# Kernel optimization log

Hardware: AMD Instinct MI355X
Metric: run time of the kernel (lower is better)

The kernel has to match this reference:

```python
import jax, jax.numpy as jnp
import numpy as np

B, SE, HD, ED, N, T = 64, 512, 1024, 512, 10000, 20
EOS_ID = 1
NEG_BIG = -1e9    # stand-in for -MAX_VAL encoder pad mask
MASK_VAL = -1e7   # logits_mask scatter value (-10000000.0 in torch)
M = HD + ED


def setup_inputs() -> dict:
    key = jax.random.key(0)
    ks = jax.random.split(key, 16)
    s = 0.02
    enc = jax.random.normal(ks[0], (B, SE, HD), jnp.float32)
    hidden = jax.random.normal(ks[1], (1, B, HD), jnp.float32)
    cell = jax.random.normal(ks[2], (1, B, HD), jnp.float32)
    text_lengths = jax.random.randint(ks[3], (B,), SE // 2, SE + 1)
    encoder_mask = jnp.arange(SE)[None, :] < text_lengths[:, None]  # [B,SE] bool
    embedding = jax.random.normal(ks[4], (N, ED), jnp.float32) * s
    # LSTM (PyTorch gate order i,f,g,o)
    w_ih = jax.random.normal(ks[5], (4 * HD, ED), jnp.float32) * s
    w_hh = jax.random.normal(ks[6], (4 * HD, HD), jnp.float32) * s
    b_ih = jnp.zeros((4 * HD,), jnp.float32)
    b_hh = jnp.zeros((4 * HD,), jnp.float32)
    # dense_net: Hd -> He
    w_q = jax.random.normal(ks[7], (HD, HD), jnp.float32) * s
    b_q = jnp.zeros((HD,), jnp.float32)
    # SelfAttentiveSum: Linear(Ed,Ed)+ReLU+Linear(Ed,1)
    w_k = jax.random.normal(ks[8], (ED, ED), jnp.float32) * s
    b_k = jnp.zeros((ED,), jnp.float32)
    w_ko = jax.random.normal(ks[9], (ED,), jnp.float32) * s
    b_ko = jnp.zeros((), jnp.float32)
    # MLP: Linear(M,M)+ReLU+Linear(M,N)
    w_m1 = jax.random.normal(ks[10], (M, M), jnp.float32) * s
    b_m1 = jnp.zeros((M,), jnp.float32)
    w_m2 = jax.random.normal(ks[11], (N, M), jnp.float32) * s
    b_m2 = jnp.zeros((N,), jnp.float32)
    return dict(encoded_hidden_embeddings=enc, hidden=hidden, cell=cell,
                text_lengths=text_lengths, encoder_mask=encoder_mask,
                embedding=embedding, w_ih=w_ih, w_hh=w_hh, b_ih=b_ih, b_hh=b_hh,
                w_q=w_q, b_q=b_q, w_k=w_k, b_k=b_k, w_ko=w_ko, b_ko=b_ko,
                w_m1=w_m1, b_m1=b_m1, w_m2=w_m2, b_m2=b_m2)


def _decode(enc, h0, c0, encoder_mask, embedding, w_ih, w_hh, b_ih, b_hh,
            w_q, b_q, w_k, b_k, w_ko, b_ko, w_m1, b_m1, w_m2, b_m2):
    pad_mask = jnp.where(encoder_mask, 0.0, NEG_BIG).astype(enc.dtype)  # [B,SE]
    sent = enc[:, 0, :]  # [B,HD] sentence representation (dropout is identity in eval)

    def step(carry, t):
        h, c, inp, logits_mask, buf = carry
        # --- LSTM cell (single step) ---
        gates = inp @ w_ih.T + b_ih + h @ w_hh.T + b_hh  # [B,4HD]
        i, f, g, o = jnp.split(gates, 4, axis=-1)
        c = jax.nn.sigmoid(f) * c + jax.nn.sigmoid(i) * jnp.tanh(g)
        h = jax.nn.sigmoid(o) * jnp.tanh(c)
        # --- attention over encoder states ---
        q = h @ w_q.T + b_q                                   # [B,HD]
        score = jnp.einsum('bsh,bh->bs', enc, q) + pad_mask    # [B,SE]
        w = jax.nn.softmax(score, axis=1)
        attn_enc = jnp.einsum('bs,bsh->bh', w, enc)            # [B,HD]
        # --- self-attentive sum over previously predicted label embeddings ---
        valid = jnp.arange(T) < jnp.maximum(t, 1)              # step 0: zeros row 0 valid
        k = jax.nn.relu(buf @ w_k.T + b_k) @ w_ko + b_ko       # [B,T]
        k = jnp.where(valid[None, :], k, NEG_BIG)
        sw = jax.nn.softmax(k, axis=1)
        attn_last = jnp.einsum('bt,bte->be', sw, buf)          # [B,ED]
        # --- MLP ---
        m = jnp.concatenate([sent + attn_enc, inp + attn_last], axis=-1)  # [B,M]
        logits = jax.nn.relu(m @ w_m1.T + b_m1) @ w_m2.T + b_m2 + logits_mask  # [B,N]
        next_ids = jnp.argmax(logits, axis=-1)                 # [B]
        pred_emb = embedding[next_ids]                          # [B,ED]
        buf = buf.at[:, t].set(pred_emb)
        logits_mask = logits_mask.at[jnp.arange(B), next_ids].set(MASK_VAL)
        logits_mask = logits_mask.at[:, EOS_ID].set(0.0)
        return (h, c, pred_emb, logits_mask, buf), (logits, next_ids)

    init = (h0, c0,
            jnp.zeros((B, ED), enc.dtype),
            jnp.zeros((B, N), enc.dtype),
            jnp.zeros((B, T, ED), enc.dtype))
    _, (outs, ids) = jax.lax.scan(step, init, jnp.arange(T))
    return jnp.transpose(outs, (1, 0, 2)), jnp.transpose(ids, (1, 0))  # [B,T,N],[B,T]


def reference(encoded_hidden_embeddings, hidden, cell, text_lengths, encoder_mask,
              embedding, w_ih, w_hh, b_ih, b_hh, w_q, b_q, w_k, b_k, w_ko, b_ko,
              w_m1, b_m1, w_m2, b_m2):
    # De=1: [1,B,HD] -> [B,HD]
    return _decode(encoded_hidden_embeddings, hidden[0], cell[0], encoder_mask,
                   embedding, w_ih, w_hh, b_ih, b_hh, w_q, b_q, w_k, b_k,
                   w_ko, b_ko, w_m1, b_m1, w_m2, b_m2)
```

## Files before the change

kernel.cpp:

```cpp
#include <hip/hip_runtime.h>

#define B64 64
#define SE 512
#define HD 1024
#define ED 512
#define NV 10000
#define TT 20
#define MM 1536
#define MASK_VALF -10000000.0f

#define OFF_XA    0
#define OFF_XB    98304
#define OFF_CT    196608
#define OFF_QF    262144
#define OFF_FM    327680
#define OFF_FL    328704
#define OFF_FACC  329728
#define OFF_XT2   1378304
#define OFF_H1T   1476608
#define OFF_ARGV  1574912
#define OFF_ARGI  1654912
#define OFF_MASKT 1734912
#define OFF_BUF   2374912
#define OFF_BUFT  3030272
#define OFF_KVP   3685632
#define OFF_LP    3767552

__device__ __forceinline__ float sigmoidf_(float x) { return 1.f / (1.f + expf(-x)); }

__global__ __launch_bounds__(256) void k_init(const float* __restrict__ h0,
                                              const float* __restrict__ c0,
                                              float* __restrict__ ws) {
  int idx = blockIdx.x * 256 + threadIdx.x, stride = gridDim.x * 256;
  float* xa = ws + OFF_XA;
  float* cT = ws + OFF_CT;
  float* maskT = ws + OFF_MASKT;
  float* buf = ws + OFF_BUF;
  float* bufT = ws + OFF_BUFT;
  for (int i = idx; i < 512 * 64; i += stride) xa[i] = 0.f;
  for (int i = idx; i < NV * 64; i += stride) maskT[i] = 0.f;
  for (int i = idx; i < B64 * TT * ED; i += stride) { buf[i] = 0.f; bufT[i] = 0.f; }
  for (int i = idx; i < HD * 64; i += stride) {
    int u = i >> 6, b = i & 63;
    xa[512 * 64 + i] = h0[b * HD + u];
    cT[i] = c0[b * HD + u];
  }
}

__global__ __launch_bounds__(256) void k_cellks(const float* __restrict__ xcur,
                                                const float* __restrict__ w_ih,
                                                const float* __restrict__ w_hh,
                                                const float* __restrict__ b_ih,
                                                const float* __restrict__ b_hh,
                                                float* __restrict__ cT,
                                                float* __restrict__ xnext,
                                                const float* __restrict__ bufT,
                                                const float* __restrict__ w_k,
                                                const float* __restrict__ b_k,
                                                const float* __restrict__ w_ko,
                                                float* __restrict__ kvp, int j) {
  __shared__ float wl[8 * 1536];
  int tid = threadIdx.x, lane = tid & 63, wid = tid >> 6;

  if (blockIdx.x >= 512) {
    int ug = blockIdx.x - 512;
    int u0 = ug * 8;
    int k0 = wid * 128;
    const float* xp = bufT + (size_t)j * 64 + lane;
    float acc[8] = {0, 0, 0, 0, 0, 0, 0, 0};
    for (int k4 = 0; k4 < 32; ++k4) {
      int e = k0 + 4 * k4;
      float x0 = xp[(size_t)(e + 0) * (TT * 64)];
      float x1 = xp[(size_t)(e + 1) * (TT * 64)];
      float x2 = xp[(size_t)(e + 2) * (TT * 64)];
      float x3 = xp[(size_t)(e + 3) * (TT * 64)];
#pragma unroll
      for (int i = 0; i < 8; ++i) {
        const float4 w4 = *(const float4*)&w_k[(size_t)(u0 + i) * 512 + e];
        acc[i] = fmaf(w4.x, x0, acc[i]);
        acc[i] = fmaf(w4.y, x1, acc[i]);
        acc[i] = fmaf(w4.z, x2, acc[i]);
        acc[i] = fmaf(w4.w, x3, acc[i]);
      }
    }
    float* sacc = wl;
#pragma unroll
    for (int i = 0; i < 8; ++i) sacc[(wid * 8 + i) * 64 + lane] = acc[i];
    __syncthreads();
    if (wid == 0) {
      float kp = 0.f;
#pragma unroll
      for (int i = 0; i < 8; ++i) {
        float tot = b_k[u0 + i] + sacc[(0 * 8 + i) * 64 + lane] + sacc[(1 * 8 + i) * 64 + lane] +
                    sacc[(2 * 8 + i) * 64 + lane] + sacc[(3 * 8 + i) * 64 + lane];
        kp += fmaxf(tot, 0.f) * w_ko[u0 + i];
      }
      kvp[((size_t)ug * TT + j) * 64 + lane] = kp;
    }
    return;
  }

  int u0 = blockIdx.x * 2;
  for (int i = tid; i < 3072; i += 256) {
    int lr = i / 384, kq = i % 384;
    int k = kq * 4;
    int grow = (lr >> 1) * 1024 + u0 + (lr & 1);
    float4 v;
    if (k < 512) v = *(const float4*)&w_ih[(size_t)grow * 512 + k];
    else v = *(const float4*)&w_hh[(size_t)grow * 1024 + (k - 512)];
    *(float4*)&wl[lr * 1536 + k] = v;
  }
  __syncthreads();
  int kbase = wid * 384;
  const float* xp = xcur + (size_t)kbase * 64 + lane;
  float acc[8] = {0, 0, 0, 0, 0, 0, 0, 0};
#pragma unroll 2
  for (int k4 = 0; k4 < 96; ++k4) {
    float x0 = xp[(4 * k4 + 0) * 64];
    float x1 = xp[(4 * k4 + 1) * 64];
    float x2 = xp[(4 * k4 + 2) * 64];
    float x3 = xp[(4 * k4 + 3) * 64];
#pragma unroll
    for (int lr = 0; lr < 8; ++lr) {
      const float4 w4 = *(const float4*)&wl[lr * 1536 + kbase + 4 * k4];
      acc[lr] = fmaf(w4.x, x0, acc[lr]);
      acc[lr] = fmaf(w4.y, x1, acc[lr]);
      acc[lr] = fmaf(w4.z, x2, acc[lr]);
      acc[lr] = fmaf(w4.w, x3, acc[lr]);
    }
  }
  __syncthreads();
#pragma unroll
  for (int lr = 0; lr < 8; ++lr) wl[wid * 512 + lr * 64 + lane] = acc[lr];
  __syncthreads();
  if (tid < 128) {
    int jj = tid >> 6, b = tid & 63;
    float g4[4];
#pragma unroll
    for (int g = 0; g < 4; ++g) {
      int lr = g * 2 + jj;
      int grow = g * 1024 + u0 + jj;
      float v = b_ih[grow] + b_hh[grow];
#pragma unroll
      for (int w = 0; w < 4; ++w) v += wl[w * 512 + lr * 64 + b];
      g4[g] = v;
    }
    int u = u0 + jj;
    float c = cT[u * 64 + b];
    float cn = sigmoidf_(g4[1]) * c + sigmoidf_(g4[0]) * tanhf(g4[2]);
    float hn = sigmoidf_(g4[3]) * tanhf(cn);
    cT[u * 64 + b] = cn;
    xnext[(512 + u) * 64 + b] = hn;
  }
}

__global__ __launch_bounds__(256) void k_q2h(const float* __restrict__ h,
                                             const float* __restrict__ w_q,
                                             const float* __restrict__ b_q,
                                             float* __restrict__ qf,
                                             const float* __restrict__ kvp,
                                             const float* __restrict__ b_ko,
                                             const float* __restrict__ buf,
                                             const float* __restrict__ inpT,
                                             float* __restrict__ xT2, int tv) {
  __shared__ float wl[8 * 1024];
  __shared__ float pw[TT];
  int tid = threadIdx.x, lane = tid & 63, wid = tid >> 6;

  if (blockIdx.x >= 128) {
    int b = blockIdx.x - 128;
    if (tid < tv) {
      float s = b_ko[0];
#pragma unroll 8
      for (int g = 0; g < 64; ++g) s += kvp[((size_t)g * TT + tid) * 64 + b];
      pw[tid] = s;
    }
    __syncthreads();
    float mx = -1e30f;
    for (int k = 0; k < tv; ++k) mx = fmaxf(mx, pw[k]);
    float den = 0.f;
    for (int k = 0; k < tv; ++k) den += expf(pw[k] - mx);
    float invd = 1.f / den;
    __syncthreads();
    if (tid < tv) pw[tid] = expf(pw[tid] - mx) * invd;
    __syncthreads();
    for (int e = tid; e < 512; e += 256) {
      float a = 0.f;
      for (int k = 0; k < tv; ++k) a += pw[k] * buf[((size_t)b * TT + k) * 512 + e];
      xT2[(1024 + e) * 64 + b] = inpT[e * 64 + b] + a;
    }
    return;
  }

  int h0 = blockIdx.x * 8;
  for (int i = tid; i < 2048; i += 256) {
    int lr = i >> 8, kq = i & 255;
    *(float4*)&wl[lr * 1024 + kq * 4] = *(const float4*)&w_q[(size_t)(h0 + lr) * 1024 + kq * 4];
  }
  __syncthreads();
  int kbase = wid * 256;
  const float* xp = h + (size_t)kbase * 64 + lane;
  float acc[8] = {0, 0, 0, 0, 0, 0, 0, 0};
#pragma unroll 2
  for (int k4 = 0; k4 < 64; ++k4) {
    float x0 = xp[(4 * k4 + 0) * 64];
    float x1 = xp[(4 * k4 + 1) * 64];
    float x2 = xp[(4 * k4 + 2) * 64];
    float x3 = xp[(4 * k4 + 3) * 64];
#pragma unroll
    for (int lr = 0; lr < 8; ++lr) {
      const float4 w4 = *(const float4*)&wl[lr * 1024 + kbase + 4 * k4];
      acc[lr] = fmaf(w4.x, x0, acc[lr]);
      acc[lr] = fmaf(w4.y, x1, acc[lr]);
      acc[lr] = fmaf(w4.z, x2, acc[lr]);
      acc[lr] = fmaf(w4.w, x3, acc[lr]);
    }
  }
  __syncthreads();
#pragma unroll
  for (int lr = 0; lr < 8; ++lr) wl[wid * 512 + lr * 64 + lane] = acc[lr];
  __syncthreads();
  for (int e = tid; e < 512; e += 256) {
    int lr = e >> 6, b = e & 63;
    float v = b_q[h0 + lr];
#pragma unroll
    for (int w = 0; w < 4; ++w) v += wl[w * 512 + lr * 64 + b];
    qf[(size_t)b * 1024 + h0 + lr] = v;
  }
}

__global__ __launch_bounds__(256) void k_flash(const float* __restrict__ enc,
                                               const int* __restrict__ tlen,
                                               const float* __restrict__ qf,
                                               float* __restrict__ fm, float* __restrict__ fl,
                                               float* __restrict__ facc) {
  __shared__ float lacc[4][1024];
  __shared__ float lml[4][2];
  int b = blockIdx.x >> 4, split = blockIdx.x & 15;
  int tid = threadIdx.x, lane = tid & 63, wid = tid >> 6;
  int len = tlen[b];
  float qv[16];
#pragma unroll
  for (int j = 0; j < 4; ++j) {
    float4 tq = *(const float4*)&qf[(size_t)b * 1024 + j * 256 + lane * 4];
    qv[4 * j + 0] = tq.x; qv[4 * j + 1] = tq.y; qv[4 * j + 2] = tq.z; qv[4 * j + 3] = tq.w;
  }
  const float* base = enc + (size_t)b * SE * HD;
  int s0 = split * 32 + wid * 8;
  int nr = len - s0;
  nr = nr < 0 ? 0 : (nr > 8 ? 8 : nr);
  int npair = nr >> 1;

  float4 cA[4], cB[4], nA[4], nB[4];
  float m = -1e30f, l = 0.f, acc[16];
#pragma unroll
  for (int j = 0; j < 16; ++j) acc[j] = 0.f;

#define LOADROW(d, s)                                                 \
  {                                                                   \
    const float4* rp = (const float4*)(base + (size_t)(s)*HD) + lane; \
    d[0] = rp[0]; d[1] = rp[64]; d[2] = rp[128]; d[3] = rp[192];      \
  }

  if (npair > 0) { LOADROW(cA, s0); LOADROW(cB, s0 + 1); }
  for (int p = 0; p < npair; ++p) {
    if (p + 1 < npair) {
      LOADROW(nA, s0 + 2 * p + 2);
      LOADROW(nB, s0 + 2 * p + 3);
    } else if (nr & 1) {
      LOADROW(nA, s0 + nr - 1);
    }
    float d0 = 0.f, d1 = 0.f;
#pragma unroll
    for (int j = 0; j < 4; ++j) {
      d0 = fmaf(qv[4 * j + 0], cA[j].x, d0); d1 = fmaf(qv[4 * j + 0], cB[j].x, d1);
      d0 = fmaf(qv[4 * j + 1], cA[j].y, d0); d1 = fmaf(qv[4 * j + 1], cB[j].y, d1);
      d0 = fmaf(qv[4 * j + 2], cA[j].z, d0); d1 = fmaf(qv[4 * j + 2], cB[j].z, d1);
      d0 = fmaf(qv[4 * j + 3], cA[j].w, d0); d1 = fmaf(qv[4 * j + 3], cB[j].w, d1);
    }
#pragma unroll
    for (int off = 32; off; off >>= 1) { d0 += __shfl_xor(d0, off, 64); d1 += __shfl_xor(d1, off, 64); }
    d0 = __shfl(d0, 0, 64);
    d1 = __shfl(d1, 0, 64);
    float mn = fmaxf(m, fmaxf(d0, d1));
    float sc = expf(m - mn), p0 = expf(d0 - mn), p1 = expf(d1 - mn);
    l = l * sc + p0 + p1;
#pragma unroll
    for (int j = 0; j < 4; ++j) {
      acc[4 * j + 0] = fmaf(p1, cB[j].x, fmaf(p0, cA[j].x, acc[4 * j + 0] * sc));
      acc[4 * j + 1] = fmaf(p1, cB[j].y, fmaf(p0, cA[j].y, acc[4 * j + 1] * sc));
      acc[4 * j + 2] = fmaf(p1, cB[j].z, fmaf(p0, cA[j].z, acc[4 * j + 2] * sc));
      acc[4 * j + 3] = fmaf(p1, cB[j].w, fmaf(p0, cA[j].w, acc[4 * j + 3] * sc));
    }
    m = mn;
#pragma unroll
    for (int j = 0; j < 4; ++j) { cA[j] = nA[j]; cB[j] = nB[j]; }
  }
  if (nr & 1) {
    if (npair == 0) LOADROW(cA, s0);
    float d0 = 0.f;
#pragma unroll
    for (int j = 0; j < 4; ++j) {
      d0 = fmaf(qv[4 * j + 0], cA[j].x, d0);
      d0 = fmaf(qv[4 * j + 1], cA[j].y, d0);
      d0 = fmaf(qv[4 * j + 2], cA[j].z, d0);
      d0 = fmaf(qv[4 * j + 3], cA[j].w, d0);
    }
#pragma unroll
    for (int off = 32; off; off >>= 1) d0 += __shfl_xor(d0, off, 64);
    d0 = __shfl(d0, 0, 64);
    float mn = fmaxf(m, d0);
    float sc = expf(m - mn), p0 = expf(d0 - mn);
    l = l * sc + p0;
#pragma unroll
    for (int j = 0; j < 4; ++j) {
      acc[4 * j + 0] = fmaf(p0, cA[j].x, acc[4 * j + 0] * sc);
      acc[4 * j + 1] = fmaf(p0, cA[j].y, acc[4 * j + 1] * sc);
      acc[4 * j + 2] = fmaf(p0, cA[j].z, acc[4 * j + 2] * sc);
      acc[4 * j + 3] = fmaf(p0, cA[j].w, acc[4 * j + 3] * sc);
    }
    m = mn;
  }
#undef LOADROW
#pragma unroll
  for (int j = 0; j < 4; ++j)
    *(float4*)&lacc[wid][j * 256 + lane * 4] =
        make_float4(acc[4 * j], acc[4 * j + 1], acc[4 * j + 2], acc[4 * j + 3]);
  if (lane == 0) { lml[wid][0] = m; lml[wid][1] = l; }
  __syncthreads();
  float M = fmaxf(fmaxf(lml[0][0], lml[1][0]), fmaxf(lml[2][0], lml[3][0]));
  float w0 = expf(lml[0][0] - M), w1 = expf(lml[1][0] - M);
  float w2 = expf(lml[2][0] - M), w3 = expf(lml[3][0] - M);
  float L = w0 * lml[0][1] + w1 * lml[1][1] + w2 * lml[2][1] + w3 * lml[3][1];
  int p = b * 16 + split;
  for (int h = tid; h < 1024; h += 256)
    facc[(size_t)p * 1024 + h] =
        w0 * lacc[0][h] + w1 * lacc[1][h] + w2 * lacc[2][h] + w3 * lacc[3][h];
  if (tid == 0) { fm[p] = M; fl[p] = L; }
}

__global__ __launch_bounds__(256) void k_ctx(const float* __restrict__ enc,
                                             const float* __restrict__ fm,
                                             const float* __restrict__ fl,
                                             const float* __restrict__ facc,
                                             float* __restrict__ xT2) {
  int b = blockIdx.x >> 2, qd = blockIdx.x & 3;
  int tid = threadIdx.x;
  float M = -1e30f;
#pragma unroll
  for (int k = 0; k < 16; ++k) M = fmaxf(M, fm[b * 16 + k]);
  float w[16];
  float L = 0.f;
#pragma unroll
  for (int k = 0; k < 16; ++k) {
    w[k] = expf(fm[b * 16 + k] - M);
    L += w[k] * fl[b * 16 + k];
  }
  float inv = 1.f / L;
  int h = qd * 256 + tid;
  float s = 0.f;
#pragma unroll
  for (int k = 0; k < 16; ++k) s += w[k] * facc[(size_t)(b * 16 + k) * 1024 + h];
  xT2[h * 64 + b] = enc[(size_t)b * SE * HD + h] + s * inv;
}

__global__ __launch_bounds__(256) void k_h12(const float* __restrict__ xT2,
                                             const float* __restrict__ w_m1,
                                             const float* __restrict__ b_m1,
                                             float* __restrict__ h1T) {
  __shared__ float wl[8 * 1536];
  int tid = threadIdx.x;
  int r0 = blockIdx.x * 8;
  for (int i = tid; i < 3072; i += 256) {
    int lr = i / 384, kq = i % 384;
    *(float4*)&wl[lr * 1536 + kq * 4] = *(const float4*)&w_m1[(size_t)(r0 + lr) * MM + kq * 4];
  }
  __syncthreads();
  int lane = tid & 63, wid = tid >> 6;
  int kbase = wid * 384;
  const float* xp = xT2 + (size_t)kbase * 64 + lane;
  float acc[8] = {0, 0, 0, 0, 0, 0, 0, 0};
#pragma unroll 2
  for (int k4 = 0; k4 < 96; ++k4) {
    float x0 = xp[(4 * k4 + 0) * 64];
    float x1 = xp[(4 * k4 + 1) * 64];
    float x2 = xp[(4 * k4 + 2) * 64];
    float x3 = xp[(4 * k4 + 3) * 64];
#pragma unroll
    for (int lr = 0; lr < 8; ++lr) {
      const float4 w4 = *(const float4*)&wl[lr * 1536 + kbase + 4 * k4];
      acc[lr] = fmaf(w4.x, x0, acc[lr]);
      acc[lr] = fmaf(w4.y, x1, acc[lr]);
      acc[lr] = fmaf(w4.z, x2, acc[lr]);
      acc[lr] = fmaf(w4.w, x3, acc[lr]);
    }
  }
  __syncthreads();
#pragma unroll
  for (int lr = 0; lr < 8; ++lr) wl[wid * 512 + lr * 64 + lane] = acc[lr];
  __syncthreads();
  for (int e = tid; e < 512; e += 256) {
    int lr = e >> 6, b = e & 63;
    float v = b_m1[r0 + lr];
#pragma unroll
    for (int w = 0; w < 4; ++w) v += wl[w * 512 + lr * 64 + b];
    h1T[(size_t)(r0 + lr) * 64 + b] = fmaxf(v, 0.f);
  }
}

__global__ __launch_bounds__(256) void k_vocab(const float* __restrict__ h1T,
                                               const float* __restrict__ w_m2,
                                               float* __restrict__ lp) {
  __shared__ float Wl[128 * 36];
  __shared__ float Xl[32 * 68];
  int tid = threadIdx.x;
  int r0b = blockIdx.x * 128;
  int k0 = blockIdx.y * 256;
  int tc = tid & 15, tr = tid >> 4;
  int r0 = tr * 8, b0 = tc * 4;
  float4 acc[8];
#pragma unroll
  for (int i = 0; i < 8; ++i) acc[i] = make_float4(0.f, 0.f, 0.f, 0.f);
  for (int kt = 0; kt < 8; ++kt) {
    int kbase = k0 + kt * 32;
#pragma unroll
    for (int j = 0; j < 4; ++j) {
      int f = tid + 256 * j;
      int row = f >> 3, kkq = (f & 7) * 4;
      int gr = r0b + row;
      if (gr > NV - 1) gr = NV - 1;
      *(float4*)&Wl[row * 36 + kkq] = *(const float4*)&w_m2[(size_t)gr * MM + kbase + kkq];
    }
#pragma unroll
    for (int j = 0; j < 2; ++j) {
      int f = tid + 256 * j;
      int kk = f >> 4, bq = (f & 15) * 4;
      *(float4*)&Xl[kk * 68 + bq] = *(const float4*)&h1T[(size_t)(kbase + kk) * 64 + bq];
    }
    __syncthreads();
#pragma unroll 2
    for (int kq = 0; kq < 8; ++kq) {
      float4 xv0 = *(const float4*)&Xl[(kq * 4 + 0) * 68 + b0];
      float4 xv1 = *(const float4*)&Xl[(kq * 4 + 1) * 68 + b0];
      float4 xv2 = *(const float4*)&Xl[(kq * 4 + 2) * 68 + b0];
      float4 xv3 = *(const float4*)&Xl[(kq * 4 + 3) * 68 + b0];
#pragma unroll
      for (int i = 0; i < 8; ++i) {
        float4 av = *(const float4*)&Wl[(r0 + i) * 36 + kq * 4];
        acc[i].x = fmaf(av.x, xv0.x, acc[i].x);
        acc[i].y = fmaf(av.x, xv0.y, acc[i].y);
        acc[i].z = fmaf(av.x, xv0.z, acc[i].z);
        acc[i].w = fmaf(av.x, xv0.w, acc[i].w);
        acc[i].x = fmaf(av.y, xv1.x, acc[i].x);
        acc[i].y = fmaf(av.y, xv1.y, acc[i].y);
        acc[i].z = fmaf(av.y, xv1.z, acc[i].z);
        acc[i].w = fmaf(av.y, xv1.w, acc[i].w);
        acc[i].x = fmaf(av.z, xv2.x, acc[i].x);
        acc[i].y = fmaf(av.z, xv2.y, acc[i].y);
        acc[i].z = fmaf(av.z, xv2.z, acc[i].z);
        acc[i].w = fmaf(av.z, xv2.w, acc[i].w);
        acc[i].x = fmaf(av.w, xv3.x, acc[i].x);
        acc[i].y = fmaf(av.w, xv3.y, acc[i].y);
        acc[i].z = fmaf(av.w, xv3.z, acc[i].z);
        acc[i].w = fmaf(av.w, xv3.w, acc[i].w);
      }
    }
    __syncthreads();
  }
  float* o = lp + (size_t)blockIdx.y * 640000;
#pragma unroll
  for (int i = 0; i < 8; ++i) {
    int r = r0b + r0 + i;
    if (r < NV) *(float4*)&o[(size_t)r * 64 + b0] = acc[i];
  }
}

__global__ __launch_bounds__(256) void k_logfin(const float* __restrict__ lp,
                                                const float* __restrict__ b_m2,
                                                const float* __restrict__ maskT,
                                                float* __restrict__ argv, int* __restrict__ argi,
                                                float* __restrict__ out, int t) {
  __shared__ float tile[32][65];
  int lane = threadIdx.x & 63, wid = threadIdx.x >> 6;
  int rg = blockIdx.x * 4 + wid;
  int nb = blockIdx.x * 32;
  if (rg < 1250) {
    int r0 = rg * 8;
    float best = -3.4e38f;
    int bi = 0;
#pragma unroll
    for (int i = 0; i < 8; ++i) {
      int r = r0 + i;
      size_t idx = (size_t)r * 64 + lane;
      float v = b_m2[r] + maskT[idx];
#pragma unroll
      for (int s = 0; s < 6; ++s) v += lp[(size_t)s * 640000 + idx];
      tile[wid * 8 + i][lane] = v;
      if (v > best) { best = v; bi = r; }
    }
    argv[(size_t)rg * 64 + lane] = best;
    argi[(size_t)rg * 64 + lane] = bi;
  }
  __syncthreads();
  int b = threadIdx.x >> 2, q = threadIdx.x & 3;
  int nloc = q * 8;
  if (nb + nloc < NV) {
    float tmp[8];
#pragma unroll
    for (int c = 0; c < 8; ++c) tmp[c] = tile[nloc + c][b];
    float4* o = (float4*)&out[((size_t)b * TT + t) * NV + nb + nloc];
    o[0] = make_float4(tmp[0], tmp[1], tmp[2], tmp[3]);
    o[1] = make_float4(tmp[4], tmp[5], tmp[6], tmp[7]);
  }
}

__global__ __launch_bounds__(256) void k_final(const float* __restrict__ argv,
                                               const int* __restrict__ argi,
                                               const float* __restrict__ emb,
                                               float* __restrict__ maskT,
                                               float* __restrict__ xnext,
                                               float* __restrict__ buf, float* __restrict__ bufT,
                                               float* __restrict__ out_ids, int t) {
  __shared__ float sv[256];
  __shared__ int si_[256];
  __shared__ int sid;
  int b = blockIdx.x, tid = threadIdx.x;
  float best = -3.4e38f;
  int bi = 0x7fffffff;
  for (int g = tid; g < 1250; g += 256) {
    float v = argv[(size_t)g * 64 + b];
    int idx = argi[(size_t)g * 64 + b];
    if (v > best || (v == best && idx < bi)) { best = v; bi = idx; }
  }
  sv[tid] = best;
  si_[tid] = bi;
  __syncthreads();
  for (int off = 128; off; off >>= 1) {
    if (tid < off) {
      float v2 = sv[tid + off];
      int i2 = si_[tid + off];
      if (v2 > sv[tid] || (v2 == sv[tid] && i2 < si_[tid])) { sv[tid] = v2; si_[tid] = i2; }
    }
    __syncthreads();
  }
  if (tid == 0) {
    sid = si_[0];
    out_ids[b * TT + t] = (float)si_[0];
    if (si_[0] != 1) maskT[(size_t)si_[0] * 64 + b] = MASK_VALF;
  }
  __syncthreads();
  int id = sid;
  for (int e = tid; e < 512; e += 256) {
    float v = emb[(size_t)id * 512 + e];
    xnext[e * 64 + b] = v;
    buf[((size_t)b * TT + t) * 512 + e] = v;
    bufT[(size_t)e * (TT * 64) + t * 64 + b] = v;
  }
}

extern "C" void kernel_launch(void* const* d_in, const int* in_sizes, int n_in,
                              void* d_out, int out_size, void* d_ws, size_t ws_size,
                              hipStream_t stream) {
  const float* enc = (const float*)d_in[0];
  const float* h0 = (const float*)d_in[1];
  const float* c0 = (const float*)d_in[2];
  const int* tlen = (const int*)d_in[3];
  const float* emb = (const float*)d_in[5];
  const float* w_ih = (const float*)d_in[6];
  const float* w_hh = (const float*)d_in[7];
  const float* b_ih = (const float*)d_in[8];
  const float* b_hh = (const float*)d_in[9];
  const float* w_q = (const float*)d_in[10];
  const float* b_q = (const float*)d_in[11];
  const float* w_k = (const float*)d_in[12];
  const float* b_k = (const float*)d_in[13];
  const float* w_ko = (const float*)d_in[14];
  const float* b_ko = (const float*)d_in[15];
  const float* w_m1 = (const float*)d_in[16];
  const float* b_m1 = (const float*)d_in[17];
  const float* w_m2 = (const float*)d_in[18];
  const float* b_m2 = (const float*)d_in[19];

  float* ws = (float*)d_ws;
  float* out_logits = (float*)d_out;
  float* out_ids = out_logits + (size_t)B64 * TT * NV;

  k_init<<<2048, 256, 0, stream>>>(h0, c0, ws);

  for (int t = 0; t < TT; ++t) {
    int tv = (t < 1) ? 1 : t;
    int jcol = (t == 0) ? 0 : t - 1;
    float* xcur = ws + ((t & 1) ? OFF_XB : OFF_XA);
    float* xnext = ws + ((t & 1) ? OFF_XA : OFF_XB);
    k_cellks<<<576, 256, 0, stream>>>(xcur, w_ih, w_hh, b_ih, b_hh, ws + OFF_CT, xnext,
                                      ws + OFF_BUFT, w_k, b_k, w_ko, ws + OFF_KVP, jcol);
    k_q2h<<<192, 256, 0, stream>>>(xnext + 512 * 64, w_q, b_q, ws + OFF_QF, ws + OFF_KVP, b_ko,
                                   ws + OFF_BUF, xcur, ws + OFF_XT2, tv);
    k_flash<<<1024, 256, 0, stream>>>(enc, tlen, ws + OFF_QF, ws + OFF_FM, ws + OFF_FL,
                                      ws + OFF_FACC);
    k_ctx<<<256, 256, 0, stream>>>(enc, ws + OFF_FM, ws + OFF_FL, ws + OFF_FACC, ws + OFF_XT2);
    k_h12<<<192, 256, 0, stream>>>(ws + OFF_XT2, w_m1, b_m1, ws + OFF_H1T);
    k_vocab<<<dim3(79, 6), 256, 0, stream>>>(ws + OFF_H1T, w_m2, ws + OFF_LP);
    k_logfin<<<313, 256, 0, stream>>>(ws + OFF_LP, b_m2, ws + OFF_MASKT, ws + OFF_ARGV,
                                      (int*)(ws + OFF_ARGI), out_logits, t);
    k_final<<<64, 256, 0, stream>>>(ws + OFF_ARGV, (int*)(ws + OFF_ARGI), emb, ws + OFF_MASKT,
                                    xnext, ws + OFF_BUF, ws + OFF_BUFT, out_ids, t);
  }
}
```

Baseline: 2.840 ms.

## Split MLP first layer and overlap the query-independent part with flash attention

The first MLP layer's dot product over the last 512 input columns (the predicted-embedding part of xT2, which k_q2h writes) is moved into extra blocks of the flash-attention kernel. It runs concurrently with the attention splits and writes partial sums to a new workspace buffer. k_h12 then only processes the first 1024 columns (the context part) and adds in the precomputed partial. This shortens the serial MLP kernel on the critical path and fills idle CUs during attention, at the cost of extra workspace traffic and an extra read per output.

After: 2.832 ms. No clear change (-0.3%).

```diff
diff --git a/kernel.cpp b/kernel.cpp
--- a/kernel.cpp
+++ b/kernel.cpp
@@ -18,13 +18,14 @@
 #define OFF_FACC  329728
 #define OFF_XT2   1378304
 #define OFF_H1T   1476608
-#define OFF_ARGV  1574912
-#define OFF_ARGI  1654912
-#define OFF_MASKT 1734912
-#define OFF_BUF   2374912
-#define OFF_BUFT  3030272
-#define OFF_KVP   3685632
-#define OFF_LP    3767552
+#define OFF_H1P2  1574912
+#define OFF_ARGV  1673216
+#define OFF_ARGI  1753216
+#define OFF_MASKT 1833216
+#define OFF_BUF   2473216
+#define OFF_BUFT  3128576
+#define OFF_KVP   3783936
+#define OFF_LP    3865856
 
 __device__ __forceinline__ float sigmoidf_(float x) { return 1.f / (1.f + expf(-x)); }
 
@@ -229,15 +230,59 @@
   }
 }
 
-__global__ __launch_bounds__(256) void k_flash(const float* __restrict__ enc,
-                                               const int* __restrict__ tlen,
-                                               const float* __restrict__ qf,
-                                               float* __restrict__ fm, float* __restrict__ fl,
-                                               float* __restrict__ facc) {
-  __shared__ float lacc[4][1024];
-  __shared__ float lml[4][2];
+__global__ __launch_bounds__(256) void k_flashh1(const float* __restrict__ enc,
+                                                 const int* __restrict__ tlen,
+                                                 const float* __restrict__ qf,
+                                                 float* __restrict__ fm, float* __restrict__ fl,
+                                                 float* __restrict__ facc,
+                                                 const float* __restrict__ xT2,
+                                                 const float* __restrict__ w_m1,
+                                                 float* __restrict__ h1p2) {
+  __shared__ float smem[4104];
+  int tid = threadIdx.x, lane = tid & 63, wid = tid >> 6;
+
+  if (blockIdx.x >= 1024) {
+    int r0 = (blockIdx.x - 1024) * 8;
+    float* wl = smem;
+    for (int i = tid; i < 1024; i += 256) {
+      int lr = i >> 7, kq = (i & 127) * 4;
+      *(float4*)&wl[lr * 512 + kq] = *(const float4*)&w_m1[(size_t)(r0 + lr) * MM + 1024 + kq];
+    }
+    __syncthreads();
+    int kbase = wid * 128;
+    const float* xp = xT2 + (size_t)(1024 + kbase) * 64 + lane;
+    float acc[8] = {0, 0, 0, 0, 0, 0, 0, 0};
+#pragma unroll 2
+    for (int k4 = 0; k4 < 32; ++k4) {
+      float x0 = xp[(4 * k4 + 0) * 64];
+      float x1 = xp[(4 * k4 + 1) * 64];
+      float x2 = xp[(4 * k4 + 2) * 64];
+      float x3 = xp[(4 * k4 + 3) * 64];
+#pragma unroll
+      for (int lr = 0; lr < 8; ++lr) {
+        const float4 w4 = *(const float4*)&wl[lr * 512 + kbase + 4 * k4];
+        acc[lr] = fmaf(w4.x, x0, acc[lr]);
+        acc[lr] = fmaf(w4.y, x1, acc[lr]);
+        acc[lr] = fmaf(w4.z, x2, acc[lr]);
+        acc[lr] = fmaf(w4.w, x3, acc[lr]);
+      }
+    }
+    __syncthreads();
+#pragma unroll
+    for (int lr = 0; lr < 8; ++lr) wl[(wid * 8 + lr) * 64 + lane] = acc[lr];
+    __syncthreads();
+    for (int e = tid; e < 512; e += 256) {
+      int lr = e >> 6, b = e & 63;
+      float v = wl[(0 * 8 + lr) * 64 + b] + wl[(1 * 8 + lr) * 64 + b] +
+                wl[(2 * 8 + lr) * 64 + b] + wl[(3 * 8 + lr) * 64 + b];
+      h1p2[(size_t)(r0 + lr) * 64 + b] = v;
+    }
+    return;
+  }
+
+  float* lacc = smem;
+  float* lml = smem + 4096;
   int b = blockIdx.x >> 4, split = blockIdx.x & 15;
-  int tid = threadIdx.x, lane = tid & 63, wid = tid >> 6;
   int len = tlen[b];
   float qv[16];
 #pragma unroll
@@ -324,18 +369,19 @@
 #undef LOADROW
 #pragma unroll
   for (int j = 0; j < 4; ++j)
-    *(float4*)&lacc[wid][j * 256 + lane * 4] =
+    *(float4*)&lacc[wid * 1024 + j * 256 + lane * 4] =
         make_float4(acc[4 * j], acc[4 * j + 1], acc[4 * j + 2], acc[4 * j + 3]);
-  if (lane == 0) { lml[wid][0] = m; lml[wid][1] = l; }
-  __syncthreads();
-  float M = fmaxf(fmaxf(lml[0][0], lml[1][0]), fmaxf(lml[2][0], lml[3][0]));
-  float w0 = expf(lml[0][0] - M), w1 = expf(lml[1][0] - M);
-  float w2 = expf(lml[2][0] - M), w3 = expf(lml[3][0] - M);
-  float L = w0 * lml[0][1] + w1 * lml[1][1] + w2 * lml[2][1] + w3 * lml[3][1];
+  if (lane == 0) { lml[wid * 2 + 0] = m; lml[wid * 2 + 1] = l; }
+  __syncthreads();
+  float M = fmaxf(fmaxf(lml[0], lml[2]), fmaxf(lml[4], lml[6]));
+  float w0 = expf(lml[0] - M), w1 = expf(lml[2] - M);
+  float w2 = expf(lml[4] - M), w3 = expf(lml[6] - M);
+  float L = w0 * lml[1] + w1 * lml[3] + w2 * lml[5] + w3 * lml[7];
   int p = b * 16 + split;
   for (int h = tid; h < 1024; h += 256)
     facc[(size_t)p * 1024 + h] =
-        w0 * lacc[0][h] + w1 * lacc[1][h] + w2 * lacc[2][h] + w3 * lacc[3][h];
+        w0 * lacc[0 * 1024 + h] + w1 * lacc[1 * 1024 + h] + w2 * lacc[2 * 1024 + h] +
+        w3 * lacc[3 * 1024 + h];
   if (tid == 0) { fm[p] = M; fl[p] = L; }
 }
 
@@ -367,28 +413,29 @@
 __global__ __launch_bounds__(256) void k_h12(const float* __restrict__ xT2,
                                              const float* __restrict__ w_m1,
                                              const float* __restrict__ b_m1,
+                                             const float* __restrict__ h1p2,
                                              float* __restrict__ h1T) {
-  __shared__ float wl[8 * 1536];
+  __shared__ float wl[8 * 1024];
   int tid = threadIdx.x;
   int r0 = blockIdx.x * 8;
-  for (int i = tid; i < 3072; i += 256) {
-    int lr = i / 384, kq = i % 384;
-    *(float4*)&wl[lr * 1536 + kq * 4] = *(const float4*)&w_m1[(size_t)(r0 + lr) * MM + kq * 4];
+  for (int i = tid; i < 2048; i += 256) {
+    int lr = i >> 8, kq = (i & 255) * 4;
+    *(float4*)&wl[lr * 1024 + kq] = *(const float4*)&w_m1[(size_t)(r0 + lr) * MM + kq];
   }
   __syncthreads();
   int lane = tid & 63, wid = tid >> 6;
-  int kbase = wid * 384;
+  int kbase = wid * 256;
   const float* xp = xT2 + (size_t)kbase * 64 + lane;
   float acc[8] = {0, 0, 0, 0, 0, 0, 0, 0};
 #pragma unroll 2
-  for (int k4 = 0; k4 < 96; ++k4) {
+  for (int k4 = 0; k4 < 64; ++k4) {
     float x0 = xp[(4 * k4 + 0) * 64];
     float x1 = xp[(4 * k4 + 1) * 64];
     float x2 = xp[(4 * k4 + 2) * 64];
     float x3 = xp[(4 * k4 + 3) * 64];
 #pragma unroll
     for (int lr = 0; lr < 8; ++lr) {
-      const float4 w4 = *(const float4*)&wl[lr * 1536 + kbase + 4 * k4];
+      const float4 w4 = *(const float4*)&wl[lr * 1024 + kbase + 4 * k4];
       acc[lr] = fmaf(w4.x, x0, acc[lr]);
       acc[lr] = fmaf(w4.y, x1, acc[lr]);
       acc[lr] = fmaf(w4.z, x2, acc[lr]);
@@ -401,7 +448,7 @@
   __syncthreads();
   for (int e = tid; e < 512; e += 256) {
     int lr = e >> 6, b = e & 63;
-    float v = b_m1[r0 + lr];
+    float v = b_m1[r0 + lr] + h1p2[(size_t)(r0 + lr) * 64 + b];
 #pragma unroll
     for (int w = 0; w < 4; ++w) v += wl[w * 512 + lr * 64 + b];
     h1T[(size_t)(r0 + lr) * 64 + b] = fmaxf(v, 0.f);
@@ -596,10 +643,10 @@
                                       ws + OFF_BUFT, w_k, b_k, w_ko, ws + OFF_KVP, jcol);
     k_q2h<<<192, 256, 0, stream>>>(xnext + 512 * 64, w_q, b_q, ws + OFF_QF, ws + OFF_KVP, b_ko,
                                    ws + OFF_BUF, xcur, ws + OFF_XT2, tv);
-    k_flash<<<1024, 256, 0, stream>>>(enc, tlen, ws + OFF_QF, ws + OFF_FM, ws + OFF_FL,
-                                      ws + OFF_FACC);
+    k_flashh1<<<1216, 256, 0, stream>>>(enc, tlen, ws + OFF_QF, ws + OFF_FM, ws + OFF_FL,
+                                        ws + OFF_FACC, ws + OFF_XT2, w_m1, ws + OFF_H1P2);
     k_ctx<<<256, 256, 0, stream>>>(enc, ws + OFF_FM, ws + OFF_FL, ws + OFF_FACC, ws + OFF_XT2);
-    k_h12<<<192, 256, 0, stream>>>(ws + OFF_XT2, w_m1, b_m1, ws + OFF_H1T);
+    k_h12<<<192, 256, 0, stream>>>(ws + OFF_XT2, w_m1, b_m1, ws + OFF_H1P2, ws + OFF_H1T);
     k_vocab<<<dim3(79, 6), 256, 0, stream>>>(ws + OFF_H1T, w_m2, ws + OFF_LP);
     k_logfin<<<313, 256, 0, stream>>>(ws + OFF_LP, b_m2, ws + OFF_MASKT, ws + OFF_ARGV,
                                       (int*)(ws + OFF_ARGI), out_logits, t);
```
